# Optimization experiments

Hardware: AMD Instinct MI355X
Metric: run time of the kernel (lower is better)

The kernel has to match this reference:

```python
import jax, jax.numpy as jnp
import numpy as np

ALPHA = 2.0
BIG = 1e10  # stands in for +inf in the min-plus EDT recurrence (avoids inf*0 NaNs)


def _edt_sq_1d_last(f):
    # Exact 1D squared-distance transform along last axis:
    #   out[i] = min_j f[j] + (i - j)^2   (Felzenszwalb-Huttenlocher lower envelope,
    #   computed here as a vectorized min-plus contraction).
    n = f.shape[-1]
    i = jnp.arange(n)
    par = ((i[:, None] - i[None, :]) ** 2).astype(f.dtype)  # [n_out, n_in]
    return jnp.min(f[..., None, :] + par, axis=-1)  # [..., n_out]


def _edt(mask):
    # Exact Euclidean distance transform over axes (1,2,3) of a [B,C,H,W] bool mask:
    # distance from each True pixel to the nearest False pixel (0 on False pixels),
    # matching scipy.ndimage.distance_transform_edt applied per-batch to img[b].
    f = jnp.where(mask, jnp.float32(BIG), jnp.float32(0.0))
    for ax in (1, 2, 3):
        f = jnp.moveaxis(_edt_sq_1d_last(jnp.moveaxis(f, ax, -1)), -1, ax)
    return jnp.sqrt(jnp.minimum(f, BIG))


def _distance_field(img):
    fg = img > 0.5
    fg_any = fg.any(axis=(1, 2, 3))  # original skips samples with empty foreground
    field = _edt(fg) + _edt(~fg)
    return jnp.where(fg_any[:, None, None, None], field, 0.0)


def setup_inputs() -> dict:
    key = jax.random.key(0)
    k1, k2 = jax.random.split(key)
    pred = jax.random.uniform(k1, (4, 1, 256, 256), dtype=jnp.float32)
    # target is a binary segmentation mask in practice
    target = (jax.random.uniform(k2, (4, 1, 256, 256)) > 0.5).astype(jnp.float32)
    return {"pred": pred, "target": target}


def reference(pred, target):
    pred_dt = jax.lax.stop_gradient(_distance_field(pred))      # computed under no_grad
    target_dt = jax.lax.stop_gradient(_distance_field(target))  # computed under no_grad
    pred_error = (pred - target) ** 2
    distance = pred_dt ** ALPHA + target_dt ** ALPHA
    return (pred_error * distance).mean()
```

## Files before the change

kernel.cpp:

```cpp
#include <hip/hip_runtime.h>

#define BIGF 1e10f
#define HH 256
#define WW 256
#define BB 4
#define NPIX (BB * HH * WW)
#define GRID 256
#define MAGIC 0x5F3A9C71u

#define WS_ACCB_OFF 0
#define WS_RDY_OFF 2048
#define WS_DONE_OFF 3072
#define WS_MASK_OFF 4096

#define LOAD_RLX(p)     __hip_atomic_load((p), __ATOMIC_RELAXED, __HIP_MEMORY_SCOPE_AGENT)
#define STORE_RLX(p, v) __hip_atomic_store((p), (v), __ATOMIC_RELAXED, __HIP_MEMORY_SCOPE_AGENT)

__device__ inline float row_d2(const unsigned* __restrict__ rm, int x, unsigned iv) {
    int wx = x >> 5, bx = x & 31;
    int dl = 1 << 20, dr = 1 << 20;
    unsigned m0 = rm[wx] ^ iv;
    unsigned t = m0 & (0xFFFFFFFFu >> (31 - bx));
    int w = wx;
    while (true) {
        if (t) { int p = (w << 5) + 31 - __builtin_clz(t); dl = x - p; break; }
        if (--w < 0) break;
        t = rm[w] ^ iv;
    }
    t = m0 & (0xFFFFFFFFu << bx);
    w = wx;
    while (true) {
        if (t) { int p = (w << 5) + __builtin_ctz(t); dr = p - x; break; }
        if (++w > 7) break;
        t = rm[w] ^ iv;
    }
    int d = dl < dr ? dl : dr;
    return (d > 255) ? BIGF : (float)(d * d);
}

__device__ inline float col_min(const unsigned* __restrict__ mb, int y, int x, unsigned iv) {
    float best = row_d2(mb + y * 8, x, iv);
    #pragma unroll 1
    for (int s = 1; s < HH; ++s) {
        float ss = (float)(s * s);
        if (ss >= best) break;
        int ym = y - s, yp = y + s;
        if (ym >= 0) best = fminf(best, row_d2(mb + ym * 8, x, iv) + ss);
        if (yp < HH) best = fminf(best, row_d2(mb + yp * 8, x, iv) + ss);
    }
    return best;
}

__launch_bounds__(1024, 4)
__global__ void hdt_kernel(const float* __restrict__ pred,
                           const float* __restrict__ tgt,
                           unsigned* __restrict__ gmask,
                           unsigned* __restrict__ ready,
                           unsigned* __restrict__ done,
                           unsigned long long* __restrict__ accb,
                           float* __restrict__ out) {
    int blk = blockIdx.x;
    int b = blk >> 6;
    int tid = threadIdx.x;
    int w = tid >> 6, lane = tid & 63;

    __shared__ __align__(16) unsigned lmask[2][HH][8];
    __shared__ unsigned wfl[16];
    __shared__ float wsum[16];
    __shared__ double dsum[4];

    int x = tid & (WW - 1);
    int yq = ((blk & 63) << 2) + (tid >> 8);
    int idx = (b * HH + yq) * WW + x;
    float pv = pred[idx], tv = tgt[idx];

    {
        int r = ((blk & 63) << 3) + (w >> 1);
        int img = r >> 8, y = r & 255, half = w & 1;
        const float* src = (img ? tgt : pred) + (b * HH + y) * WW + half * 128 + lane;
        unsigned long long b0 = __ballot(src[0] > 0.5f);
        unsigned long long b1 = __ballot(src[64] > 0.5f);
        if (lane == 0) {
            unsigned long long* dst = (unsigned long long*)
                (gmask + ((img * BB + b) * HH + y) * 8 + half * 4);
            STORE_RLX(dst, b0);
            STORE_RLX(dst + 1, b1);
        }
    }
    __syncthreads();
    if (tid == 0) STORE_RLX(&ready[blk], MAGIC);

    if (tid < 64) {
        while (LOAD_RLX(&ready[(b << 6) + tid]) != MAGIC)
            __builtin_amdgcn_s_sleep(2);
    }
    __syncthreads();

    {
        int img = tid >> 9;
        int row = (tid >> 1) & 255;
        int half = tid & 1;
        const unsigned long long* gp = (const unsigned long long*)
            (gmask + ((img * BB + b) * HH + row) * 8 + half * 4);
        unsigned long long v0 = LOAD_RLX(gp);
        unsigned long long v1 = LOAD_RLX(gp + 1);
        uint4 a = make_uint4((unsigned)v0, (unsigned)(v0 >> 32),
                             (unsigned)v1, (unsigned)(v1 >> 32));
        ((uint4*)lmask)[tid] = a;
        unsigned onz = a.x | a.y | a.z | a.w;
        unsigned long long bal = __ballot(onz != 0u);
        if ((tid & 63) == 0) wfl[tid >> 6] = (bal != 0ULL) ? 1u : 0u;
    }
    __syncthreads();
    unsigned fl_p = wfl[0] | wfl[1] | wfl[2] | wfl[3] | wfl[4] | wfl[5] | wfl[6] | wfl[7];
    unsigned fl_t = wfl[8] | wfl[9] | wfl[10] | wfl[11] | wfl[12] | wfl[13] | wfl[14] | wfl[15];

    float e = pv - tv;
    float errsq = e * e;
    float d2p = 0.0f, d2t = 0.0f;
    if (fl_p) {
        unsigned iv = (pv > 0.5f) ? 0xFFFFFFFFu : 0u;
        float best = col_min(&lmask[0][0][0], yq, x, iv);
        float dt = sqrtf(fminf(best, BIGF));
        d2p = dt * dt;
    }
    if (fl_t) {
        unsigned iv = (tv > 0.5f) ? 0xFFFFFFFFu : 0u;
        float best = col_min(&lmask[1][0][0], yq, x, iv);
        float dt = sqrtf(fminf(best, BIGF));
        d2t = dt * dt;
    }
    float lsum = errsq * (d2p + d2t);

    #pragma unroll
    for (int off = 32; off > 0; off >>= 1)
        lsum += __shfl_down(lsum, off, 64);
    if ((tid & 63) == 0) wsum[tid >> 6] = lsum;
    __syncthreads();

    if (tid == 0) {
        float s2 = 0.0f;
        #pragma unroll
        for (int i = 0; i < 16; ++i) s2 += wsum[i];
        STORE_RLX(&accb[blk], (unsigned long long)__double_as_longlong((double)s2));
        asm volatile("s_waitcnt vmcnt(0)" ::: "memory");
        STORE_RLX(&done[blk], MAGIC);
    }
    if (blk == 0) {
        double v = 0.0;
        if (tid < GRID) {
            while (LOAD_RLX(&done[tid]) != MAGIC)
                __builtin_amdgcn_s_sleep(2);
            v = __longlong_as_double((long long)LOAD_RLX(&accb[tid]));
        }
        #pragma unroll
        for (int off = 32; off > 0; off >>= 1)
            v += __shfl_down(v, off, 64);
        if (tid < GRID && (tid & 63) == 0) dsum[tid >> 6] = v;
        __syncthreads();
        if (tid == 0)
            out[0] = (float)((dsum[0] + dsum[1] + dsum[2] + dsum[3])
                             * (1.0 / (double)NPIX));
    }
}

extern "C" void kernel_launch(void* const* d_in, const int* in_sizes, int n_in,
                              void* d_out, int out_size, void* d_ws, size_t ws_size,
                              hipStream_t stream) {
    const float* pred = (const float*)d_in[0];
    const float* tgt = (const float*)d_in[1];
    float* out = (float*)d_out;
    char* ws = (char*)d_ws;
    unsigned long long* accb = (unsigned long long*)(ws + WS_ACCB_OFF);
    unsigned* ready = (unsigned*)(ws + WS_RDY_OFF);
    unsigned* done = (unsigned*)(ws + WS_DONE_OFF);
    unsigned* gmask = (unsigned*)(ws + WS_MASK_OFF);

    hdt_kernel<<<GRID, 1024, 0, stream>>>(pred, tgt, gmask, ready, done, accb, out);
}
```

Baseline: 63.87 us.

## Compute distances from local row window, skip inter-block barrier when converged

Each block now builds its own shared-memory bitmask for the rows within SMAX of its tile, loading them directly from global with float4 reads and shuffle-OR packing. It then computes a windowed column-min distance for every pixel. Only if some pixel's distance exceeds the convergence threshold does the block wait on the cross-block ready flags and load the full image mask for an exact fallback. This aims to remove the grid-wide spin-wait and the full-mask reload in the common case, at the cost of redundant per-block mask construction and a second code path that duplicates the original logic.

```diff
diff --git a/kernel.cpp b/kernel.cpp
--- a/kernel.cpp
+++ b/kernel.cpp
@@ -7,6 +7,8 @@
 #define NPIX (BB * HH * WW)
 #define GRID 256
 #define MAGIC 0x5F3A9C71u
+#define SMAX 16
+#define CONV_T 289.0f
 
 #define WS_ACCB_OFF 0
 #define WS_RDY_OFF 2048
@@ -42,6 +44,19 @@
     float best = row_d2(mb + y * 8, x, iv);
     #pragma unroll 1
     for (int s = 1; s < HH; ++s) {
+        float ss = (float)(s * s);
+        if (ss >= best) break;
+        int ym = y - s, yp = y + s;
+        if (ym >= 0) best = fminf(best, row_d2(mb + ym * 8, x, iv) + ss);
+        if (yp < HH) best = fminf(best, row_d2(mb + yp * 8, x, iv) + ss);
+    }
+    return best;
+}
+
+__device__ inline float col_min_win(const unsigned* __restrict__ mb, int y, int x, unsigned iv) {
+    float best = row_d2(mb + y * 8, x, iv);
+    #pragma unroll 1
+    for (int s = 1; s <= SMAX; ++s) {
         float ss = (float)(s * s);
         if (ss >= best) break;
         int ym = y - s, yp = y + s;
@@ -70,7 +85,8 @@
     __shared__ double dsum[4];
 
     int x = tid & (WW - 1);
-    int yq = ((blk & 63) << 2) + (tid >> 8);
+    int y0 = (blk & 63) << 2;
+    int yq = y0 + (tid >> 8);
     int idx = (b * HH + yq) * WW + x;
     float pv = pred[idx], tv = tgt[idx];
 
@@ -87,50 +103,89 @@
             STORE_RLX(dst + 1, b1);
         }
     }
+
+    int ylo = y0 - SMAX; if (ylo < 0) ylo = 0;
+    int yhi = y0 + 3 + SMAX; if (yhi > HH - 1) yhi = HH - 1;
+    int nrows = yhi - ylo + 1;
+    int tot = nrows * 2;
+    #pragma unroll 2
+    for (int i = w; i < tot; i += 16) {
+        int img = (i >= nrows) ? 1 : 0;
+        int y = ylo + (img ? i - nrows : i);
+        const float* rowp = (img ? tgt : pred) + (b * HH + y) * WW;
+        const float4 f = ((const float4*)rowp)[lane];
+        unsigned nib = (f.x > 0.5f ? 1u : 0u) | (f.y > 0.5f ? 2u : 0u)
+                     | (f.z > 0.5f ? 4u : 0u) | (f.w > 0.5f ? 8u : 0u);
+        unsigned v = nib << ((lane & 7) << 2);
+        v |= __shfl_xor(v, 1, 64);
+        v |= __shfl_xor(v, 2, 64);
+        v |= __shfl_xor(v, 4, 64);
+        if ((lane & 7) == 0) lmask[img][y][lane >> 3] = v;
+    }
     __syncthreads();
     if (tid == 0) STORE_RLX(&ready[blk], MAGIC);
 
-    if (tid < 64) {
-        while (LOAD_RLX(&ready[(b << 6) + tid]) != MAGIC)
-            __builtin_amdgcn_s_sleep(2);
-    }
+    unsigned ivp = (pv > 0.5f) ? 0xFFFFFFFFu : 0u;
+    unsigned ivt = (tv > 0.5f) ? 0xFFFFFFFFu : 0u;
+    float bp = col_min_win(&lmask[0][0][0], yq, x, ivp);
+    float bt = col_min_win(&lmask[1][0][0], yq, x, ivt);
+    bool conv_p = (bp <= CONV_T), conv_t = (bt <= CONV_T);
+    float d2p = 0.0f, d2t = 0.0f;
+    if (conv_p) { float dt = sqrtf(fminf(bp, BIGF)); d2p = dt * dt; }
+    if (conv_t) { float dt = sqrtf(fminf(bt, BIGF)); d2t = dt * dt; }
+
+    unsigned long long fb = __ballot(!(conv_p && conv_t));
+    if ((tid & 63) == 0) wfl[w] = (fb != 0ULL) ? 1u : 0u;
     __syncthreads();
-
-    {
-        int img = tid >> 9;
-        int row = (tid >> 1) & 255;
-        int half = tid & 1;
-        const unsigned long long* gp = (const unsigned long long*)
-            (gmask + ((img * BB + b) * HH + row) * 8 + half * 4);
-        unsigned long long v0 = LOAD_RLX(gp);
-        unsigned long long v1 = LOAD_RLX(gp + 1);
-        uint4 a = make_uint4((unsigned)v0, (unsigned)(v0 >> 32),
-                             (unsigned)v1, (unsigned)(v1 >> 32));
-        ((uint4*)lmask)[tid] = a;
-        unsigned onz = a.x | a.y | a.z | a.w;
-        unsigned long long bal = __ballot(onz != 0u);
-        if ((tid & 63) == 0) wfl[tid >> 6] = (bal != 0ULL) ? 1u : 0u;
-    }
-    __syncthreads();
-    unsigned fl_p = wfl[0] | wfl[1] | wfl[2] | wfl[3] | wfl[4] | wfl[5] | wfl[6] | wfl[7];
-    unsigned fl_t = wfl[8] | wfl[9] | wfl[10] | wfl[11] | wfl[12] | wfl[13] | wfl[14] | wfl[15];
+    unsigned fb_any = wfl[0] | wfl[1] | wfl[2] | wfl[3] | wfl[4] | wfl[5] | wfl[6]
+                    | wfl[7] | wfl[8] | wfl[9] | wfl[10] | wfl[11] | wfl[12]
+                    | wfl[13] | wfl[14] | wfl[15];
+
+    if (fb_any) {
+        __syncthreads();
+        if (tid < 64) {
+            while (LOAD_RLX(&ready[(b << 6) + tid]) != MAGIC)
+                __builtin_amdgcn_s_sleep(2);
+        }
+        __syncthreads();
+        {
+            int img = tid >> 9;
+            int row = (tid >> 1) & 255;
+            int half = tid & 1;
+            const unsigned long long* gp = (const unsigned long long*)
+                (gmask + ((img * BB + b) * HH + row) * 8 + half * 4);
+            unsigned long long v0 = LOAD_RLX(gp);
+            unsigned long long v1 = LOAD_RLX(gp + 1);
+            uint4 a = make_uint4((unsigned)v0, (unsigned)(v0 >> 32),
+                                 (unsigned)v1, (unsigned)(v1 >> 32));
+            ((uint4*)lmask)[tid] = a;
+            unsigned onz = a.x | a.y | a.z | a.w;
+            unsigned long long bal = __ballot(onz != 0u);
+            if ((tid & 63) == 0) wfl[tid >> 6] = (bal != 0ULL) ? 1u : 0u;
+        }
+        __syncthreads();
+        unsigned fl_p = wfl[0] | wfl[1] | wfl[2] | wfl[3] | wfl[4] | wfl[5] | wfl[6] | wfl[7];
+        unsigned fl_t = wfl[8] | wfl[9] | wfl[10] | wfl[11] | wfl[12] | wfl[13] | wfl[14] | wfl[15];
+        if (!conv_p) {
+            d2p = 0.0f;
+            if (fl_p) {
+                float best = col_min(&lmask[0][0][0], yq, x, ivp);
+                float dt = sqrtf(fminf(best, BIGF));
+                d2p = dt * dt;
+            }
+        }
+        if (!conv_t) {
+            d2t = 0.0f;
+            if (fl_t) {
+                float best = col_min(&lmask[1][0][0], yq, x, ivt);
+                float dt = sqrtf(fminf(best, BIGF));
+                d2t = dt * dt;
+            }
+        }
+    }
 
     float e = pv - tv;
-    float errsq = e * e;
-    float d2p = 0.0f, d2t = 0.0f;
-    if (fl_p) {
-        unsigned iv = (pv > 0.5f) ? 0xFFFFFFFFu : 0u;
-        float best = col_min(&lmask[0][0][0], yq, x, iv);
-        float dt = sqrtf(fminf(best, BIGF));
-        d2p = dt * dt;
-    }
-    if (fl_t) {
-        unsigned iv = (tv > 0.5f) ? 0xFFFFFFFFu : 0u;
-        float best = col_min(&lmask[1][0][0], yq, x, iv);
-        float dt = sqrtf(fminf(best, BIGF));
-        d2t = dt * dt;
-    }
-    float lsum = errsq * (d2p + d2t);
+    float lsum = (e * e) * (d2p + d2t);
 
     #pragma unroll
     for (int off = 32; off > 0; off >>= 1)
```

After: 62.81 us. About the same (-1.7%).
